# Kernel tuning notes

Measured on AMD Instinct MI355X. Metric: run time of the kernel, lower is better.

## Reference

```python
import jax, jax.numpy as jnp
import numpy as np

N = 50000          # num nodes
E = 800000         # num edges (before self-loops)
F_IN = 128         # num_node_features
HEADS = 8          # num_heads (layer 1)
F_HEAD = 16        # features_per_head
N_CLASSES = 32     # num_classes (layer 2, heads=1)
NEG_SLOPE = 0.2    # PyG GATConv default LeakyReLU slope


def setup_inputs() -> dict:
    key = jax.random.key(0)
    ks = jax.random.split(key, 9)
    x = jax.random.normal(ks[0], (N, F_IN), jnp.float32)
    src = jax.random.randint(ks[1], (E,), 0, N, dtype=jnp.int32)
    dst = jax.random.randint(ks[2], (E,), 0, N, dtype=jnp.int32)
    # layer 1 params
    W1 = jax.random.normal(ks[3], (F_IN, HEADS * F_HEAD), jnp.float32) / np.sqrt(F_IN).astype(np.float32)
    a_src1 = jax.random.normal(ks[4], (HEADS, F_HEAD), jnp.float32) * 0.1
    a_dst1 = jax.random.normal(ks[5], (HEADS, F_HEAD), jnp.float32) * 0.1
    b1 = jnp.zeros((HEADS * F_HEAD,), jnp.float32)  # bias_init = zeros_
    # layer 2 params (heads=1)
    W2 = jax.random.normal(ks[6], (HEADS * F_HEAD, N_CLASSES), jnp.float32) / np.sqrt(HEADS * F_HEAD).astype(np.float32)
    a_src2 = jax.random.normal(ks[7], (1, N_CLASSES), jnp.float32) * 0.1
    a_dst2 = jax.random.normal(ks[8], (1, N_CLASSES), jnp.float32) * 0.1
    b2 = jnp.zeros((N_CLASSES,), jnp.float32)
    return {"x": x, "src": src, "dst": dst,
            "W1": W1, "a_src1": a_src1, "a_dst1": a_dst1, "b1": b1,
            "W2": W2, "a_src2": a_src2, "a_dst2": a_dst2, "b2": b2}


def gat_conv(x, src, dst, W, a_src, a_dst, b, heads, feat):
    """PyG-style GATConv (concat=True, add_self_loops=True)."""
    h = (x @ W).reshape(N, heads, feat)                 # [N,H,F]
    al_src = jnp.sum(h * a_src, axis=-1)                # [N,H]
    al_dst = jnp.sum(h * a_dst, axis=-1)                # [N,H]
    loop = jnp.arange(N, dtype=src.dtype)
    s = jnp.concatenate([src, loop])                    # [E+N]
    d = jnp.concatenate([dst, loop])                    # [E+N]
    e = jax.nn.leaky_relu(al_src[s] + al_dst[d], NEG_SLOPE)   # [E+N,H]
    # numerically stable softmax over edges grouped by dst node
    m = jax.ops.segment_max(e, d, num_segments=N)       # [N,H]
    ex = jnp.exp(e - m[d])
    denom = jax.ops.segment_sum(ex, d, num_segments=N)  # [N,H]
    alpha = ex / denom[d]                               # [E+N,H]
    out = jax.ops.segment_sum(alpha[:, :, None] * h[s], d, num_segments=N)  # [N,H,F]
    return out.reshape(N, heads * feat) + b


def reference(x, src, dst, W1, a_src1, a_dst1, b1, W2, a_src2, a_dst2, b2):
    h = gat_conv(x, src, dst, W1, a_src1, a_dst1, b1, HEADS, F_HEAD)
    h = jax.nn.elu(h)
    h = gat_conv(h, src, dst, W2, a_src2, a_dst2, b2, 1, N_CLASSES)
    return jax.nn.log_softmax(h, axis=1)
```

## Files before the change

### kernel.cpp

```cpp
#include <hip/hip_runtime.h>

#define N_NODES   50000
#define N_EDGES   800000
#define NEG_SLOPE 0.2f
#define NBKT      256
#define NPB       196
#define EPB       3125
#define CAP       4096
#define G1BLK     782

typedef float f32x2 __attribute__((ext_vector_type(2)));
typedef float f32x4 __attribute__((ext_vector_type(4)));

__device__ __forceinline__ float leaky(float x) {
    return x > 0.f ? x : x * NEG_SLOPE;
}

__device__ __forceinline__ unsigned short f2bf(float f) {
    unsigned int u = __float_as_uint(f);
    unsigned int r = (u + 0x7FFFu + ((u >> 16) & 1u)) >> 16;
    return (unsigned short)r;
}

__device__ __forceinline__ unsigned int pack2bf(float a, float b) {
    return (unsigned int)f2bf(a) | ((unsigned int)f2bf(b) << 16);
}

__device__ __forceinline__ f32x2 bf2x2(unsigned int p) {
    f32x2 r;
    r.x = __uint_as_float(p << 16);
    r.y = __uint_as_float(p & 0xFFFF0000u);
    return r;
}

__device__ __forceinline__ f32x2 lo2(f32x4 v) { return __builtin_shufflevector(v, v, 0, 1); }
__device__ __forceinline__ f32x2 hi2(f32x4 v) { return __builtin_shufflevector(v, v, 2, 3); }

__device__ __forceinline__ void pkfma_lo(f32x2& acc, f32x2 a, f32x2 w) {
    asm("v_pk_fma_f32 %0, %1, %2, %0 op_sel:[0,0,0] op_sel_hi:[0,1,1]"
        : "+v"(acc) : "v"(a), "v"(w));
}
__device__ __forceinline__ void pkfma_hi(f32x2& acc, f32x2 a, f32x2 w) {
    asm("v_pk_fma_f32 %0, %1, %2, %0 op_sel:[1,0,0] op_sel_hi:[1,1,1]"
        : "+v"(acc) : "v"(a), "v"(w));
}
__device__ __forceinline__ f32x2 plow(float x) {
    f32x2 r;
    asm("" : "=v"(r));
    r.x = x;
    return r;
}

__global__ __launch_bounds__(256) void k_bin_gemm1(
    const int* __restrict__ src, const int* __restrict__ dst,
    int* __restrict__ cursor_g, unsigned int* __restrict__ binned,
    const float* __restrict__ x, const float* __restrict__ W1,
    const float* __restrict__ a_src, const float* __restrict__ a_dst,
    unsigned short* __restrict__ h1b, float* __restrict__ al_src,
    float* __restrict__ al_dst)
{
    __shared__ __align__(16) unsigned char smem[49152];
    const int tid = threadIdx.x;

    if (blockIdx.x < NBKT) {
        int* dstc = (int*)smem;
        int* cnt  = (int*)(smem + 12512);
        int* cur  = (int*)(smem + 13536);
        const int blk = blockIdx.x;
        const int e0  = blk * EPB;
        cnt[tid] = 0;
        __syncthreads();
        for (int j = tid; j < EPB; j += 256) {
            int d = dst[e0 + j];
            dstc[j] = d;
            atomicAdd(&cnt[d / NPB], 1);
        }
        __syncthreads();
        const int c = cnt[tid];
        int base = c ? atomicAdd(&cursor_g[tid], c) : 0;
        cur[tid] = tid * CAP + base;
        __syncthreads();
        for (int j = tid; j < EPB; j += 256) {
            int d   = dstc[j];
            int bkt = d / NPB;
            int dl  = d - bkt * NPB;
            int pos = atomicAdd(&cur[bkt], 1);
            binned[pos] = (unsigned int)src[e0 + j] | ((unsigned int)dl << 18);
        }
        return;
    }

    uint2* xs = (uint2*)smem;
    uint2* ws = (uint2*)(smem + 16384);
    const int bid  = (int)blockIdx.x - NBKT;
    const int row0 = bid * 64;
    const int tc   = tid & 31;
    const int tr   = tid >> 5;
    const float4* x4  = (const float4*)x;
    const float4* W14 = (const float4*)W1;

    #pragma unroll
    for (int p = 0; p < 8; ++p) {
        int i = tid + p * 256;
        int r = i >> 5, g = i & 31;
        int gr = row0 + r; if (gr > N_NODES - 1) gr = N_NODES - 1;
        float4 v = x4[gr * 32 + g];
        xs[r * 32 + g] = make_uint2(pack2bf(v.x, v.y), pack2bf(v.z, v.w));
    }
    #pragma unroll
    for (int p = 0; p < 16; ++p) {
        int i = tid + p * 256;
        int k = i >> 5, cg = i & 31;
        float4 v = W14[k * 32 + cg];
        ws[k * 32 + cg] = make_uint2(pack2bf(v.x, v.y), pack2bf(v.z, v.w));
    }
    __syncthreads();

    f32x2 acc[8][2];
    #pragma unroll
    for (int i = 0; i < 8; ++i) {
        acc[i][0] = (f32x2){0.f, 0.f};
        acc[i][1] = (f32x2){0.f, 0.f};
    }

    for (int k4 = 0; k4 < 32; ++k4) {
        f32x2 aP[8][2];
        #pragma unroll
        for (int i = 0; i < 8; ++i) {
            uint2 q = xs[(tr * 8 + i) * 32 + k4];
            aP[i][0] = bf2x2(q.x);
            aP[i][1] = bf2x2(q.y);
        }
        #pragma unroll
        for (int kk = 0; kk < 4; ++kk) {
            uint2 qw = ws[(k4 * 4 + kk) * 32 + tc];
            f32x2 wlo = bf2x2(qw.x);
            f32x2 whi = bf2x2(qw.y);
            #pragma unroll
            for (int i = 0; i < 8; ++i) {
                f32x2 ap = aP[i][kk >> 1];
                if ((kk & 1) == 0) {
                    pkfma_lo(acc[i][0], ap, wlo);
                    pkfma_lo(acc[i][1], ap, whi);
                } else {
                    pkfma_hi(acc[i][0], ap, wlo);
                    pkfma_hi(acc[i][1], ap, whi);
                }
            }
        }
    }

    const int head = tc >> 2;
    const float4 as4 = ((const float4*)a_src)[tc];
    const float4 ad4 = ((const float4*)a_dst)[tc];
    #pragma unroll
    for (int i = 0; i < 8; ++i) {
        int r = row0 + tr * 8 + i;
        float s = acc[i][0].x * as4.x + acc[i][0].y * as4.y
                + acc[i][1].x * as4.z + acc[i][1].y * as4.w;
        float d = acc[i][0].x * ad4.x + acc[i][0].y * ad4.y
                + acc[i][1].x * ad4.z + acc[i][1].y * ad4.w;
        s += __shfl_xor(s, 1); s += __shfl_xor(s, 2);
        d += __shfl_xor(d, 1); d += __shfl_xor(d, 2);
        if (r < N_NODES) {
            ((uint2*)h1b)[r * 32 + tc] =
                make_uint2(pack2bf(acc[i][0].x, acc[i][0].y),
                           pack2bf(acc[i][1].x, acc[i][1].y));
            if ((tc & 3) == 0) {
                al_src[r * 8 + head] = s;
                al_dst[r * 8 + head] = d;
            }
        }
    }
}

__global__ __launch_bounds__(1024) void k_csr_fine(const unsigned int* __restrict__ binned,
                                                   const int* __restrict__ cursor_g,
                                                   int* __restrict__ row_beg,
                                                   int* __restrict__ row_end,
                                                   int* __restrict__ csr) {
    __shared__ int cnt[256];
    __shared__ int cur[256];
    __shared__ int wsum[4];
    const int b = blockIdx.x, tid = threadIdx.x;
    const int start = b * CAP;
    const int nE    = cursor_g[b];
    if (tid < 256) cnt[tid] = 0;
    __syncthreads();
    for (int j = tid; j < nE; j += 1024)
        atomicAdd(&cnt[(binned[start + j] >> 18) & 255], 1);
    __syncthreads();
    int v = 0;
    if (tid < 256) v = cnt[tid];
    int sv = v;
    #pragma unroll
    for (int off = 1; off < 64; off <<= 1) {
        int t = __shfl_up(sv, off);
        if ((tid & 63) >= off) sv += t;
    }
    if (tid < 256 && (tid & 63) == 63) wsum[tid >> 6] = sv;
    __syncthreads();
    if (tid < 256) {
        int w = tid >> 6;
        int add = 0;
        #pragma unroll
        for (int i = 0; i < 3; ++i) add += (i < w) ? wsum[i] : 0;
        int excl = sv + add - v;
        cur[tid] = excl;
        const int node = b * NPB + tid;
        if (tid < NPB && node < N_NODES) {
            row_beg[node] = start + excl;
            row_end[node] = start + excl + v;
        }
    }
    __syncthreads();
    for (int j = tid; j < nE; j += 1024) {
        unsigned int p = binned[start + j];
        int dl  = (p >> 18) & 255;
        int pos = start + atomicAdd(&cur[dl], 1);
        csr[pos] = (int)(p & 0x3FFFFu);
    }
}

__global__ __launch_bounds__(256) void k_agg1g2(
    const unsigned short* __restrict__ h1b, const float* __restrict__ al_src,
    const float* __restrict__ al_dst, const int* __restrict__ row_beg,
    const int* __restrict__ row_end, const int* __restrict__ csr_src,
    const float* __restrict__ b1, const float* __restrict__ W2,
    const float* __restrict__ a_src2, const float* __restrict__ a_dst2,
    unsigned short* __restrict__ t2b, float* __restrict__ alS2,
    float* __restrict__ alD2)
{
    __shared__ __align__(16) float w2s[128 * 32];
    __shared__ __align__(16) float h2row[4][128];
    const int tid  = threadIdx.x;
    const int wv   = tid >> 6;
    const int n    = blockIdx.x * 4 + wv;
    const int l    = tid & 63;
    const int slot = l >> 4;
    const int f2   = l & 15;
    const int head = f2 >> 1;
    const uint4* h1q = (const uint4*)h1b;

    float4 wreg[4];
    {
        const float4* W2v = (const float4*)W2;
        #pragma unroll
        for (int p = 0; p < 4; ++p) wreg[p] = W2v[tid + p * 256];
    }
    const float alD = al_dst[n * 8 + head];
    const int beg = row_beg[n], end = row_end[n];
    {
        float4* w2sv = (float4*)w2s;
        #pragma unroll
        for (int p = 0; p < 4; ++p) {
            int g = tid + p * 256;
            w2sv[g ^ ((g >> 7) & 7)] = wreg[p];
        }
    }
    __syncthreads();

    float denom = 0.f;
    f32x2 a01 = {0.f, 0.f}, a23 = {0.f, 0.f}, a45 = {0.f, 0.f}, a67 = {0.f, 0.f};

    if (slot == 0) {
        float w = __expf(leaky(al_src[n * 8 + head] + alD));
        uint4 q = h1q[n * 16 + f2];
        denom = w;
        f32x2 wp = plow(w);
        pkfma_lo(a01, wp, bf2x2(q.x));
        pkfma_lo(a23, wp, bf2x2(q.y));
        pkfma_lo(a45, wp, bf2x2(q.z));
        pkfma_lo(a67, wp, bf2x2(q.w));
    }

    for (int j = beg + slot; j < end; j += 16) {
        const int e1 = (j + 4  < end) ? j + 4  : j;
        const int e2 = (j + 8  < end) ? j + 8  : j;
        const int e3 = (j + 12 < end) ? j + 12 : j;
        int s0 = csr_src[j];
        int s1 = csr_src[e1];
        int s2 = csr_src[e2];
        int s3 = csr_src[e3];
        float l0 = al_src[s0 * 8 + head];
        float l1 = al_src[s1 * 8 + head];
        float l2 = al_src[s2 * 8 + head];
        float l3 = al_src[s3 * 8 + head];
        uint4 q0 = h1q[s0 * 16 + f2];
        uint4 q1 = h1q[s1 * 16 + f2];
        uint4 q2 = h1q[s2 * 16 + f2];
        uint4 q3 = h1q[s3 * 16 + f2];
        float w0 = __expf(leaky(l0 + alD));
        float w1 = __expf(leaky(l1 + alD)); w1 = (e1 != j) ? w1 : 0.f;
        float w2 = __expf(leaky(l2 + alD)); w2 = (e2 != j) ? w2 : 0.f;
        float w3 = __expf(leaky(l3 + alD)); w3 = (e3 != j) ? w3 : 0.f;
        denom += (w0 + w1) + (w2 + w3);
        f32x2 wA; wA.x = w0; wA.y = w1;
        f32x2 wB; wB.x = w2; wB.y = w3;
        pkfma_lo(a01, wA, bf2x2(q0.x));
        pkfma_lo(a23, wA, bf2x2(q0.y));
        pkfma_lo(a45, wA, bf2x2(q0.z));
        pkfma_lo(a67, wA, bf2x2(q0.w));
        pkfma_hi(a01, wA, bf2x2(q1.x));
        pkfma_hi(a23, wA, bf2x2(q1.y));
        pkfma_hi(a45, wA, bf2x2(q1.z));
        pkfma_hi(a67, wA, bf2x2(q1.w));
        pkfma_lo(a01, wB, bf2x2(q2.x));
        pkfma_lo(a23, wB, bf2x2(q2.y));
        pkfma_lo(a45, wB, bf2x2(q2.z));
        pkfma_lo(a67, wB, bf2x2(q2.w));
        pkfma_hi(a01, wB, bf2x2(q3.x));
        pkfma_hi(a23, wB, bf2x2(q3.y));
        pkfma_hi(a45, wB, bf2x2(q3.z));
        pkfma_hi(a67, wB, bf2x2(q3.w));
    }

    #pragma unroll
    for (int off = 16; off <= 32; off <<= 1) {
        a01.x += __shfl_xor(a01.x, off); a01.y += __shfl_xor(a01.y, off);
        a23.x += __shfl_xor(a23.x, off); a23.y += __shfl_xor(a23.y, off);
        a45.x += __shfl_xor(a45.x, off); a45.y += __shfl_xor(a45.y, off);
        a67.x += __shfl_xor(a67.x, off); a67.y += __shfl_xor(a67.y, off);
        denom += __shfl_xor(denom, off);
    }

    {
        const float4 bA = ((const float4*)b1)[f2 * 2];
        const float4 bB = ((const float4*)b1)[f2 * 2 + 1];
        float inv = 1.f / denom;
        float o[8];
        o[0] = a01.x * inv + bA.x; o[1] = a01.y * inv + bA.y;
        o[2] = a23.x * inv + bA.z; o[3] = a23.y * inv + bA.w;
        o[4] = a45.x * inv + bB.x; o[5] = a45.y * inv + bB.y;
        o[6] = a67.x * inv + bB.z; o[7] = a67.y * inv + bB.w;
        #pragma unroll
        for (int i = 0; i < 8; ++i) o[i] = o[i] > 0.f ? o[i] : expm1f(o[i]);
        if (slot == 0) {
            *(float4*)&h2row[wv][f2 * 8]     = make_float4(o[0], o[1], o[2], o[3]);
            *(float4*)&h2row[wv][f2 * 8 + 4] = make_float4(o[4], o[5], o[6], o[7]);
        }
    }

    const int cg = l & 7;
    const int kg = l >> 3;
    const float* hrow = h2row[wv];
    f32x4 hv[4];
    #pragma unroll
    for (int t = 0; t < 4; ++t)
        hv[t] = *(const f32x4*)&hrow[kg * 16 + t * 4];
    const f32x4* w2v = (const f32x4*)w2s;
    f32x2 s01 = {0.f, 0.f}, s23 = {0.f, 0.f};
    #pragma unroll
    for (int t = 0; t < 4; ++t) {
        f32x2 hlo = lo2(hv[t]);
        f32x2 hhi = hi2(hv[t]);
        #pragma unroll
        for (int u = 0; u < 4; ++u) {
            const int k = kg * 16 + t * 4 + u;
            f32x4 w4 = w2v[(k * 8 + cg) ^ kg];
            f32x2 wlo = lo2(w4);
            f32x2 whi = hi2(w4);
            if (u == 0)      { pkfma_lo(s01, hlo, wlo); pkfma_lo(s23, hlo, whi); }
            else if (u == 1) { pkfma_hi(s01, hlo, wlo); pkfma_hi(s23, hlo, whi); }
            else if (u == 2) { pkfma_lo(s01, hhi, wlo); pkfma_lo(s23, hhi, whi); }
            else             { pkfma_hi(s01, hhi, wlo); pkfma_hi(s23, hhi, whi); }
        }
    }
    #pragma unroll
    for (int off = 8; off <= 32; off <<= 1) {
        s01.x += __shfl_xor(s01.x, off); s01.y += __shfl_xor(s01.y, off);
        s23.x += __shfl_xor(s23.x, off); s23.y += __shfl_xor(s23.y, off);
    }

    if (l < 8)
        ((uint2*)t2b)[n * 8 + cg] =
            make_uint2(pack2bf(s01.x, s01.y), pack2bf(s23.x, s23.y));

    const float4 as2 = ((const float4*)a_src2)[cg];
    const float4 ad2 = ((const float4*)a_dst2)[cg];
    float s2 = s01.x * as2.x + s01.y * as2.y + s23.x * as2.z + s23.y * as2.w;
    float d2 = s01.x * ad2.x + s01.y * ad2.y + s23.x * ad2.z + s23.y * ad2.w;
    #pragma unroll
    for (int off = 1; off <= 4; off <<= 1) {
        s2 += __shfl_xor(s2, off);
        d2 += __shfl_xor(d2, off);
    }
    if (l == 0) {
        alS2[n] = s2;
        alD2[n] = d2;
    }
}

__global__ __launch_bounds__(256) void k_agg2(
    const unsigned short* __restrict__ t2b, const float* __restrict__ al_src,
    const float* __restrict__ al_dst, const int* __restrict__ row_beg,
    const int* __restrict__ row_end, const int* __restrict__ csr_src,
    const float* __restrict__ b2, float* __restrict__ out)
{
    const int n = blockIdx.x * 4 + (threadIdx.x >> 6);
    const int l = threadIdx.x & 63;
    const int slot = l >> 3;
    const int f4   = l & 7;
    const uint2* t2u = (const uint2*)t2b;

    const float alD = al_dst[n];
    const int beg = row_beg[n], end = row_end[n];
    float denom = 0.f;
    f32x2 a01 = {0.f, 0.f}, a23 = {0.f, 0.f};
    if (slot == 0) {
        float w = __expf(leaky(al_src[n] + alD));
        uint2 q = t2u[n * 8 + f4];
        denom = w;
        f32x2 wp = plow(w);
        pkfma_lo(a01, wp, bf2x2(q.x));
        pkfma_lo(a23, wp, bf2x2(q.y));
    }
    for (int j = beg + slot; j < end; j += 32) {
        const int e1 = (j + 8  < end) ? j + 8  : j;
        const int e2 = (j + 16 < end) ? j + 16 : j;
        const int e3 = (j + 24 < end) ? j + 24 : j;
        int s0 = csr_src[j];
        int s1 = csr_src[e1];
        int s2 = csr_src[e2];
        int s3 = csr_src[e3];
        float l0 = al_src[s0];
        float l1 = al_src[s1];
        float l2 = al_src[s2];
        float l3 = al_src[s3];
        uint2 q0 = t2u[s0 * 8 + f4];
        uint2 q1 = t2u[s1 * 8 + f4];
        uint2 q2 = t2u[s2 * 8 + f4];
        uint2 q3 = t2u[s3 * 8 + f4];
        float w0 = __expf(leaky(l0 + alD));
        float w1 = __expf(leaky(l1 + alD)); w1 = (e1 != j) ? w1 : 0.f;
        float w2 = __expf(leaky(l2 + alD)); w2 = (e2 != j) ? w2 : 0.f;
        float w3 = __expf(leaky(l3 + alD)); w3 = (e3 != j) ? w3 : 0.f;
        denom += (w0 + w1) + (w2 + w3);
        f32x2 wA; wA.x = w0; wA.y = w1;
        f32x2 wB; wB.x = w2; wB.y = w3;
        pkfma_lo(a01, wA, bf2x2(q0.x));
        pkfma_lo(a23, wA, bf2x2(q0.y));
        pkfma_hi(a01, wA, bf2x2(q1.x));
        pkfma_hi(a23, wA, bf2x2(q1.y));
        pkfma_lo(a01, wB, bf2x2(q2.x));
        pkfma_lo(a23, wB, bf2x2(q2.y));
        pkfma_hi(a01, wB, bf2x2(q3.x));
        pkfma_hi(a23, wB, bf2x2(q3.y));
    }
    #pragma unroll
    for (int off = 8; off <= 32; off <<= 1) {
        a01.x += __shfl_xor(a01.x, off); a01.y += __shfl_xor(a01.y, off);
        a23.x += __shfl_xor(a23.x, off); a23.y += __shfl_xor(a23.y, off);
        denom += __shfl_xor(denom, off);
    }

    const float4 bb = ((const float4*)b2)[f4];
    float inv = 1.f / denom;
    float o0 = a01.x * inv + bb.x;
    float o1 = a01.y * inv + bb.y;
    float o2 = a23.x * inv + bb.z;
    float o3 = a23.y * inv + bb.w;
    float m = fmaxf(fmaxf(o0, o1), fmaxf(o2, o3));
    for (int off = 1; off <= 4; off <<= 1) m = fmaxf(m, __shfl_xor(m, off));
    float ssum = __expf(o0 - m) + __expf(o1 - m) + __expf(o2 - m) + __expf(o3 - m);
    for (int off = 1; off <= 4; off <<= 1) ssum += __shfl_xor(ssum, off);
    float lg = m + __logf(ssum);
    if (slot == 0)
        ((float4*)out)[n * 8 + f4] = make_float4(o0 - lg, o1 - lg, o2 - lg, o3 - lg);
}

extern "C" void kernel_launch(void* const* d_in, const int* in_sizes, int n_in,
                              void* d_out, int out_size, void* d_ws, size_t ws_size,
                              hipStream_t stream) {
    const float* x      = (const float*)d_in[0];
    const int*   src    = (const int*)d_in[1];
    const int*   dst    = (const int*)d_in[2];
    const float* W1     = (const float*)d_in[3];
    const float* a_src1 = (const float*)d_in[4];
    const float* a_dst1 = (const float*)d_in[5];
    const float* b1     = (const float*)d_in[6];
    const float* W2     = (const float*)d_in[7];
    const float* a_src2 = (const float*)d_in[8];
    const float* a_dst2 = (const float*)d_in[9];
    const float* b2     = (const float*)d_in[10];
    float* out = (float*)d_out;

    char* ws = (char*)d_ws;
    size_t off = 0;
    auto alloc = [&](size_t bytes) {
        void* p = ws + off;
        off += (bytes + 255) & ~(size_t)255;
        return p;
    };
    unsigned short* h1b = (unsigned short*)alloc((size_t)N_NODES * 128 * 2);
    unsigned short* t2b = (unsigned short*)alloc((size_t)N_NODES * 32 * 2);
    float* alS1    = (float*)alloc((size_t)N_NODES * 8 * 4);
    float* alD1    = (float*)alloc((size_t)N_NODES * 8 * 4);
    float* alS2    = (float*)alloc((size_t)N_NODES * 4);
    float* alD2    = (float*)alloc((size_t)N_NODES * 4);
    int*   row_beg = (int*)alloc((size_t)N_NODES * 4);
    int*   row_end = (int*)alloc((size_t)N_NODES * 4);
    int*   csr     = (int*)alloc((size_t)NBKT * CAP * 4);
    unsigned int* binned = (unsigned int*)alloc((size_t)NBKT * CAP * 4);
    int*   cursor  = (int*)alloc((size_t)NBKT * 4);
    (void)ws_size; (void)in_sizes; (void)n_in; (void)out_size;

    hipMemsetAsync(cursor, 0, (size_t)NBKT * 4, stream);
    k_bin_gemm1<<<NBKT + G1BLK, 256, 0, stream>>>(
        src, dst, cursor, binned,
        x, W1, a_src1, a_dst1, h1b, alS1, alD1);
    k_csr_fine<<<NBKT, 1024, 0, stream>>>(binned, cursor, row_beg, row_end, csr);
    k_agg1g2<<<N_NODES / 4, 256, 0, stream>>>(
        h1b, alS1, alD1, row_beg, row_end, csr,
        b1, W2, a_src2, a_dst2, t2b, alS2, alD2);
    k_agg2<<<N_NODES / 4, 256, 0, stream>>>(t2b, alS2, alD2, row_beg, row_end, csr, b2, out);
}
```

Before: 202.0 us.

## Split layer-1 aggregation and layer-2 GEMM into separate kernels

Unfuses the layer-2 projection from the layer-1 aggregation kernel. The aggregation now writes ELU outputs as fp32 to a new workspace buffer, and a new GEMM kernel processes 32 nodes per block with W2 fragments held in registers. The aim is to stop reloading W2 (16 KB) into shared memory for every 4-node block and to shrink the aggregation kernel's shared-memory footprint to raise occupancy. In exchange it adds a launch and a 25.6 MB fp32 write plus read round trip through global memory.

Result: slower. 209.1 us (+3.5%).

```diff
diff --git a/kernel.cpp b/kernel.cpp
--- a/kernel.cpp
+++ b/kernel.cpp
@@ -8,6 +8,7 @@
 #define EPB       3125
 #define CAP       4096
 #define G1BLK     782
+#define G2BLK     1563
 
 typedef float f32x2 __attribute__((ext_vector_type(2)));
 typedef float f32x4 __attribute__((ext_vector_type(4)));
@@ -222,17 +223,12 @@
     }
 }
 
-__global__ __launch_bounds__(256) void k_agg1g2(
+__global__ __launch_bounds__(256) void k_agg1(
     const unsigned short* __restrict__ h1b, const float* __restrict__ al_src,
     const float* __restrict__ al_dst, const int* __restrict__ row_beg,
     const int* __restrict__ row_end, const int* __restrict__ csr_src,
-    const float* __restrict__ b1, const float* __restrict__ W2,
-    const float* __restrict__ a_src2, const float* __restrict__ a_dst2,
-    unsigned short* __restrict__ t2b, float* __restrict__ alS2,
-    float* __restrict__ alD2)
+    const float* __restrict__ b1, float* __restrict__ h2f)
 {
-    __shared__ __align__(16) float w2s[128 * 32];
-    __shared__ __align__(16) float h2row[4][128];
     const int tid  = threadIdx.x;
     const int wv   = tid >> 6;
     const int n    = blockIdx.x * 4 + wv;
@@ -242,23 +238,8 @@
     const int head = f2 >> 1;
     const uint4* h1q = (const uint4*)h1b;
 
-    float4 wreg[4];
-    {
-        const float4* W2v = (const float4*)W2;
-        #pragma unroll
-        for (int p = 0; p < 4; ++p) wreg[p] = W2v[tid + p * 256];
-    }
     const float alD = al_dst[n * 8 + head];
     const int beg = row_beg[n], end = row_end[n];
-    {
-        float4* w2sv = (float4*)w2s;
-        #pragma unroll
-        for (int p = 0; p < 4; ++p) {
-            int g = tid + p * 256;
-            w2sv[g ^ ((g >> 7) & 7)] = wreg[p];
-        }
-    }
-    __syncthreads();
 
     float denom = 0.f;
     f32x2 a01 = {0.f, 0.f}, a23 = {0.f, 0.f}, a45 = {0.f, 0.f}, a67 = {0.f, 0.f};
@@ -328,66 +309,116 @@
         const float4 bA = ((const float4*)b1)[f2 * 2];
         const float4 bB = ((const float4*)b1)[f2 * 2 + 1];
         float inv = 1.f / denom;
-        float o[8];
-        o[0] = a01.x * inv + bA.x; o[1] = a01.y * inv + bA.y;
-        o[2] = a23.x * inv + bA.z; o[3] = a23.y * inv + bA.w;
-        o[4] = a45.x * inv + bB.x; o[5] = a45.y * inv + bB.y;
-        o[6] = a67.x * inv + bB.z; o[7] = a67.y * inv + bB.w;
-        #pragma unroll
-        for (int i = 0; i < 8; ++i) o[i] = o[i] > 0.f ? o[i] : expm1f(o[i]);
-        if (slot == 0) {
-            *(float4*)&h2row[wv][f2 * 8]     = make_float4(o[0], o[1], o[2], o[3]);
-            *(float4*)&h2row[wv][f2 * 8 + 4] = make_float4(o[4], o[5], o[6], o[7]);
-        }
-    }
-
-    const int cg = l & 7;
-    const int kg = l >> 3;
-    const float* hrow = h2row[wv];
-    f32x4 hv[4];
+        float o0 = a01.x * inv + bA.x, o1 = a01.y * inv + bA.y;
+        float o2 = a23.x * inv + bA.z, o3 = a23.y * inv + bA.w;
+        float o4 = a45.x * inv + bB.x, o5 = a45.y * inv + bB.y;
+        float o6 = a67.x * inv + bB.z, o7 = a67.y * inv + bB.w;
+        o0 = o0 > 0.f ? o0 : expm1f(o0); o1 = o1 > 0.f ? o1 : expm1f(o1);
+        o2 = o2 > 0.f ? o2 : expm1f(o2); o3 = o3 > 0.f ? o3 : expm1f(o3);
+        o4 = o4 > 0.f ? o4 : expm1f(o4); o5 = o5 > 0.f ? o5 : expm1f(o5);
+        o6 = o6 > 0.f ? o6 : expm1f(o6); o7 = o7 > 0.f ? o7 : expm1f(o7);
+        if (slot < 2) {
+            float4 v = (slot == 0) ? make_float4(o0, o1, o2, o3)
+                                   : make_float4(o4, o5, o6, o7);
+            ((float4*)h2f)[n * 32 + f2 * 2 + slot] = v;
+        }
+    }
+}
+
+__global__ __launch_bounds__(256) void k_gemm2(
+    const float* __restrict__ h2f, const float* __restrict__ W2,
+    const float* __restrict__ a_src2, const float* __restrict__ a_dst2,
+    unsigned short* __restrict__ t2b, float* __restrict__ alS2,
+    float* __restrict__ alD2)
+{
+    __shared__ __align__(16) float w2s[128 * 32];
+    __shared__ __align__(16) float h2s[32 * 128];
+    const int tid = threadIdx.x;
+    const int wv  = tid >> 6;
+    const int l   = tid & 63;
+    const int cg  = l & 7;
+    const int kg  = l >> 3;
+    const int nbase = blockIdx.x * 32;
+
+    {
+        const float4* W2v = (const float4*)W2;
+        float4* w2sv = (float4*)w2s;
+        #pragma unroll
+        for (int p = 0; p < 4; ++p) {
+            int g = tid + p * 256;
+            w2sv[g ^ ((g >> 7) & 7)] = W2v[g];
+        }
+    }
+    {
+        const float4* hv4 = (const float4*)h2f;
+        float4* hsv = (float4*)h2s;
+        #pragma unroll
+        for (int p = 0; p < 4; ++p) {
+            int g = tid + p * 256;
+            int row = g >> 5;
+            int grow = nbase + row; if (grow > N_NODES - 1) grow = N_NODES - 1;
+            hsv[g] = hv4[grow * 32 + (g & 31)];
+        }
+    }
+    __syncthreads();
+
+    const f32x4* w2v = (const f32x4*)w2s;
+    f32x4 wf[16];
     #pragma unroll
     for (int t = 0; t < 4; ++t)
-        hv[t] = *(const f32x4*)&hrow[kg * 16 + t * 4];
-    const f32x4* w2v = (const f32x4*)w2s;
-    f32x2 s01 = {0.f, 0.f}, s23 = {0.f, 0.f};
-    #pragma unroll
-    for (int t = 0; t < 4; ++t) {
-        f32x2 hlo = lo2(hv[t]);
-        f32x2 hhi = hi2(hv[t]);
         #pragma unroll
         for (int u = 0; u < 4; ++u) {
-            const int k = kg * 16 + t * 4 + u;
-            f32x4 w4 = w2v[(k * 8 + cg) ^ kg];
-            f32x2 wlo = lo2(w4);
-            f32x2 whi = hi2(w4);
-            if (u == 0)      { pkfma_lo(s01, hlo, wlo); pkfma_lo(s23, hlo, whi); }
-            else if (u == 1) { pkfma_hi(s01, hlo, wlo); pkfma_hi(s23, hlo, whi); }
-            else if (u == 2) { pkfma_lo(s01, hhi, wlo); pkfma_lo(s23, hhi, whi); }
-            else             { pkfma_hi(s01, hhi, wlo); pkfma_hi(s23, hhi, whi); }
-        }
-    }
-    #pragma unroll
-    for (int off = 8; off <= 32; off <<= 1) {
-        s01.x += __shfl_xor(s01.x, off); s01.y += __shfl_xor(s01.y, off);
-        s23.x += __shfl_xor(s23.x, off); s23.y += __shfl_xor(s23.y, off);
-    }
-
-    if (l < 8)
-        ((uint2*)t2b)[n * 8 + cg] =
-            make_uint2(pack2bf(s01.x, s01.y), pack2bf(s23.x, s23.y));
-
+            int k = kg * 16 + t * 4 + u;
+            wf[t * 4 + u] = w2v[(k * 8 + cg) ^ kg];
+        }
     const float4 as2 = ((const float4*)a_src2)[cg];
     const float4 ad2 = ((const float4*)a_dst2)[cg];
-    float s2 = s01.x * as2.x + s01.y * as2.y + s23.x * as2.z + s23.y * as2.w;
-    float d2 = s01.x * ad2.x + s01.y * ad2.y + s23.x * ad2.z + s23.y * ad2.w;
-    #pragma unroll
-    for (int off = 1; off <= 4; off <<= 1) {
-        s2 += __shfl_xor(s2, off);
-        d2 += __shfl_xor(d2, off);
-    }
-    if (l == 0) {
-        alS2[n] = s2;
-        alD2[n] = d2;
+
+    #pragma unroll 2
+    for (int m = 0; m < 8; ++m) {
+        const int n = nbase + wv * 8 + m;
+        const float* hrow = &h2s[(wv * 8 + m) * 128];
+        f32x4 hv[4];
+        #pragma unroll
+        for (int t = 0; t < 4; ++t)
+            hv[t] = *(const f32x4*)&hrow[kg * 16 + t * 4];
+        f32x2 s01 = {0.f, 0.f}, s23 = {0.f, 0.f};
+        #pragma unroll
+        for (int t = 0; t < 4; ++t) {
+            f32x2 hlo = lo2(hv[t]);
+            f32x2 hhi = hi2(hv[t]);
+            #pragma unroll
+            for (int u = 0; u < 4; ++u) {
+                f32x4 w4 = wf[t * 4 + u];
+                f32x2 wlo = lo2(w4);
+                f32x2 whi = hi2(w4);
+                if (u == 0)      { pkfma_lo(s01, hlo, wlo); pkfma_lo(s23, hlo, whi); }
+                else if (u == 1) { pkfma_hi(s01, hlo, wlo); pkfma_hi(s23, hlo, whi); }
+                else if (u == 2) { pkfma_lo(s01, hhi, wlo); pkfma_lo(s23, hhi, whi); }
+                else             { pkfma_hi(s01, hhi, wlo); pkfma_hi(s23, hhi, whi); }
+            }
+        }
+        #pragma unroll
+        for (int off = 8; off <= 32; off <<= 1) {
+            s01.x += __shfl_xor(s01.x, off); s01.y += __shfl_xor(s01.y, off);
+            s23.x += __shfl_xor(s23.x, off); s23.y += __shfl_xor(s23.y, off);
+        }
+        if (n < N_NODES) {
+            if (l < 8)
+                ((uint2*)t2b)[n * 8 + cg] =
+                    make_uint2(pack2bf(s01.x, s01.y), pack2bf(s23.x, s23.y));
+            float s2 = s01.x * as2.x + s01.y * as2.y + s23.x * as2.z + s23.y * as2.w;
+            float d2 = s01.x * ad2.x + s01.y * ad2.y + s23.x * ad2.z + s23.y * ad2.w;
+            #pragma unroll
+            for (int off = 1; off <= 4; off <<= 1) {
+                s2 += __shfl_xor(s2, off);
+                d2 += __shfl_xor(d2, off);
+            }
+            if (l == 0) {
+                alS2[n] = s2;
+                alD2[n] = d2;
+            }
+        }
     }
 }
 
@@ -494,6 +525,7 @@
     };
     unsigned short* h1b = (unsigned short*)alloc((size_t)N_NODES * 128 * 2);
     unsigned short* t2b = (unsigned short*)alloc((size_t)N_NODES * 32 * 2);
+    float* h2f     = (float*)alloc((size_t)N_NODES * 128 * 4);
     float* alS1    = (float*)alloc((size_t)N_NODES * 8 * 4);
     float* alD1    = (float*)alloc((size_t)N_NODES * 8 * 4);
     float* alS2    = (float*)alloc((size_t)N_NODES * 4);
@@ -510,8 +542,9 @@
         src, dst, cursor, binned,
         x, W1, a_src1, a_dst1, h1b, alS1, alD1);
     k_csr_fine<<<NBKT, 1024, 0, stream>>>(binned, cursor, row_beg, row_end, csr);
-    k_agg1g2<<<N_NODES / 4, 256, 0, stream>>>(
-        h1b, alS1, alD1, row_beg, row_end, csr,
-        b1, W2, a_src2, a_dst2, t2b, alS2, alD2);
+    k_agg1<<<N_NODES / 4, 256, 0, stream>>>(
+        h1b, alS1, alD1, row_beg, row_end, csr, b1, h2f);
+    k_gemm2<<<G2BLK, 256, 0, stream>>>(
+        h2f, W2, a_src2, a_dst2, t2b, alS2, alD2);
     k_agg2<<<N_NODES / 4, 256, 0, stream>>>(t2b, alS2, alD2, row_beg, row_end, csr, b2, out);
 }
```
